# Kernel optimization log

Hardware: AMD Instinct MI355X
Metric: run time of the kernel (lower is better)

The kernel has to match this reference:

```python
import jax, jax.numpy as jnp
import numpy as np

S, T, BERT, POS = 256, 512, 768, 128
H1 = 1024
NUM_CLASSES = 6


def setup_inputs() -> dict:
    key = jax.random.key(0)
    ks = jax.random.split(key, 12)
    emb = jax.random.normal(ks[0], (S, T, BERT), dtype=jnp.float32)
    pos = jax.random.normal(ks[1], (S, T, POS), dtype=jnp.float32)
    seg = jnp.sort(jax.random.randint(ks[2], (S,), 0, 64)).astype(jnp.int32)
    scale = 0.02
    return {
        "embeddings": emb,
        "position_encodings": pos,
        "W_attn": jax.random.normal(ks[3], (BERT + POS, 1), dtype=jnp.float32) * scale,
        "b_attn": jnp.zeros((1,), dtype=jnp.float32),
        "W1": jax.random.normal(ks[4], (BERT, H1), dtype=jnp.float32) * scale,
        "b1": jnp.zeros((H1,), dtype=jnp.float32),
        "W2": jax.random.normal(ks[5], (H1, H1), dtype=jnp.float32) * scale,
        "b2": jnp.zeros((H1,), dtype=jnp.float32),
        "W3": jax.random.normal(ks[6], (H1, NUM_CLASSES), dtype=jnp.float32) * scale,
        "b3": jnp.zeros((NUM_CLASSES,), dtype=jnp.float32),
        "segment_ids": seg,
        "num_comments": 64,
    }


def reference(embeddings, position_encodings, W_attn, b_attn, W1, b1, W2, b2, W3, b3, segment_ids, num_comments):
    # attention logits: Linear(bert+pos -> 1) over concatenated features, shape (S, T, 1)
    attn = jnp.concatenate([embeddings, position_encodings], axis=2) @ W_attn + b_attn
    # per-segment softmax over the 512-token dim (torch Softmax(1) on (b-a, 512, 1))
    w = jax.nn.softmax(attn, axis=1)
    # softmax-weighted pooling per segment -> (S, BERT)
    segvec = jnp.sum(w * embeddings, axis=1)
    # ragged sum over each comment's segments (contiguous bounds == sorted segment ids)
    vecs = jax.ops.segment_sum(segvec, segment_ids, num_segments=num_comments)
    # MLP head with LeakyReLU (torch default slope 0.01) and Sigmoid
    h = jax.nn.leaky_relu(vecs @ W1 + b1, negative_slope=0.01)
    h = jax.nn.leaky_relu(h @ W2 + b2, negative_slope=0.01)
    return jax.nn.sigmoid(h @ W3 + b3)
```

## Files before the change

### kernel.cpp

```cpp
#include <hip/hip_runtime.h>
#include <math.h>
#include <stdint.h>

#define S_SEQ 256
#define T_TOK 512
#define BERT 768
#define POSD 128
#define H1 1024
#define NC 6

#define CHUNK_T 128
#define WTOK 32

__global__ __launch_bounds__(256, 4) void pool_kernel(
    const float* __restrict__ emb, const float* __restrict__ pos,
    const float* __restrict__ Wa, const float* __restrict__ ba,
    float* __restrict__ part_acc, float* __restrict__ part_ml)
{
    __shared__ float mg[4 * BERT];
    __shared__ float wml[8];

    const int tid = threadIdx.x;
    const int w   = tid >> 6;
    const int l   = tid & 63;
    const int b   = blockIdx.x;
    const int s   = b >> 2;
    const int t0  = (b & 3) * CHUNK_T + w * WTOK;

    const float4* Wa4 = (const float4*)Wa;
    const float4 wa0 = Wa4[l];
    const float4 wa1 = Wa4[64 + l];
    const float4 wa2 = Wa4[128 + l];
    const float2 wp  = ((const float2*)(Wa + BERT))[l];
    const float  bav = ba[0];

    const float4* erow = (const float4*)(emb + ((size_t)s * T_TOK + t0) * BERT);
    const float2* prow = (const float2*)(pos + ((size_t)s * T_TOK + t0) * POSD);

    float m = -INFINITY, lsum = 0.f;
    float acc[12];
    #pragma unroll
    for (int j = 0; j < 12; ++j) acc[j] = 0.f;

    for (int i = 0; i < WTOK; i += 2) {
        const float4* r0 = erow + i * (BERT / 4);
        const float4* r1 = r0 + (BERT / 4);
        const float4 a0 = r0[l], a1 = r0[64 + l], a2 = r0[128 + l];
        const float4 b0 = r1[l], b1 = r1[64 + l], b2 = r1[128 + l];
        const float2 q0 = prow[i * (POSD / 2) + l];
        const float2 q1 = prow[(i + 1) * (POSD / 2) + l];

        float d0 = a0.x*wa0.x + a0.y*wa0.y + a0.z*wa0.z + a0.w*wa0.w
                 + a1.x*wa1.x + a1.y*wa1.y + a1.z*wa1.z + a1.w*wa1.w
                 + a2.x*wa2.x + a2.y*wa2.y + a2.z*wa2.z + a2.w*wa2.w
                 + q0.x*wp.x  + q0.y*wp.y;
        float d1 = b0.x*wa0.x + b0.y*wa0.y + b0.z*wa0.z + b0.w*wa0.w
                 + b1.x*wa1.x + b1.y*wa1.y + b1.z*wa1.z + b1.w*wa1.w
                 + b2.x*wa2.x + b2.y*wa2.y + b2.z*wa2.z + b2.w*wa2.w
                 + q1.x*wp.x  + q1.y*wp.y;
        #pragma unroll
        for (int off = 32; off >= 1; off >>= 1) {
            d0 += __shfl_xor(d0, off, 64);
            d1 += __shfl_xor(d1, off, 64);
        }

        const float lg0 = d0 + bav;
        const float lg1 = d1 + bav;
        const float mn  = fmaxf(m, fmaxf(lg0, lg1));
        const float alpha = __expf(m - mn);
        const float p0 = __expf(lg0 - mn);
        const float p1 = __expf(lg1 - mn);
        lsum = lsum * alpha + p0 + p1;
        m = mn;

        acc[0]  = fmaf(p0, a0.x, fmaf(p1, b0.x, acc[0]  * alpha));
        acc[1]  = fmaf(p0, a0.y, fmaf(p1, b0.y, acc[1]  * alpha));
        acc[2]  = fmaf(p0, a0.z, fmaf(p1, b0.z, acc[2]  * alpha));
        acc[3]  = fmaf(p0, a0.w, fmaf(p1, b0.w, acc[3]  * alpha));
        acc[4]  = fmaf(p0, a1.x, fmaf(p1, b1.x, acc[4]  * alpha));
        acc[5]  = fmaf(p0, a1.y, fmaf(p1, b1.y, acc[5]  * alpha));
        acc[6]  = fmaf(p0, a1.z, fmaf(p1, b1.z, acc[6]  * alpha));
        acc[7]  = fmaf(p0, a1.w, fmaf(p1, b1.w, acc[7]  * alpha));
        acc[8]  = fmaf(p0, a2.x, fmaf(p1, b2.x, acc[8]  * alpha));
        acc[9]  = fmaf(p0, a2.y, fmaf(p1, b2.y, acc[9]  * alpha));
        acc[10] = fmaf(p0, a2.z, fmaf(p1, b2.z, acc[10] * alpha));
        acc[11] = fmaf(p0, a2.w, fmaf(p1, b2.w, acc[11] * alpha));
    }

    #pragma unroll
    for (int j = 0; j < 4; ++j) {
        mg[w * BERT +       l * 4 + j] = acc[j];
        mg[w * BERT + 256 + l * 4 + j] = acc[4 + j];
        mg[w * BERT + 512 + l * 4 + j] = acc[8 + j];
    }
    if (l == 0) { wml[w * 2] = m; wml[w * 2 + 1] = lsum; }
    __syncthreads();

    const float m0 = wml[0], l0 = wml[1], m1 = wml[2], l1 = wml[3];
    const float m2 = wml[4], l2 = wml[5], m3 = wml[6], l3 = wml[7];
    const float M  = fmaxf(fmaxf(m0, m1), fmaxf(m2, m3));
    const float e0 = __expf(m0 - M), e1 = __expf(m1 - M);
    const float e2 = __expf(m2 - M), e3 = __expf(m3 - M);
    const float lt = l0 * e0 + l1 * e1 + l2 * e2 + l3 * e3;
    #pragma unroll
    for (int k = 0; k < 3; ++k) {
        const int col = tid * 3 + k;
        part_acc[(size_t)b * BERT + col] =
              e0 * mg[col] + e1 * mg[BERT + col]
            + e2 * mg[2 * BERT + col] + e3 * mg[3 * BERT + col];
    }
    if (tid == 0) { part_ml[b * 2] = M; part_ml[b * 2 + 1] = lt; }
}

__global__ void combine_segsum(
    const float* __restrict__ part_acc, const float* __restrict__ part_ml,
    const int* __restrict__ seg, float* __restrict__ vecs)
{
    const int c = blockIdx.x;
    const int tid = threadIdx.x;
    float v0 = 0.f, v1 = 0.f, v2 = 0.f;
    for (int s = 0; s < S_SEQ; ++s) {
        if (seg[s] != c) continue;
        const int p = s * 4;
        const float m0 = part_ml[(p+0)*2], l0 = part_ml[(p+0)*2+1];
        const float m1 = part_ml[(p+1)*2], l1 = part_ml[(p+1)*2+1];
        const float m2 = part_ml[(p+2)*2], l2 = part_ml[(p+2)*2+1];
        const float m3 = part_ml[(p+3)*2], l3 = part_ml[(p+3)*2+1];
        const float M  = fmaxf(fmaxf(m0, m1), fmaxf(m2, m3));
        const float e0 = __expf(m0 - M), e1 = __expf(m1 - M);
        const float e2 = __expf(m2 - M), e3 = __expf(m3 - M);
        const float inv = 1.0f / (l0*e0 + l1*e1 + l2*e2 + l3*e3);
        const int col = tid * 3;
        v0 += inv * (e0 * part_acc[(size_t)(p+0)*BERT + col]
                   + e1 * part_acc[(size_t)(p+1)*BERT + col]
                   + e2 * part_acc[(size_t)(p+2)*BERT + col]
                   + e3 * part_acc[(size_t)(p+3)*BERT + col]);
        v1 += inv * (e0 * part_acc[(size_t)(p+0)*BERT + col + 1]
                   + e1 * part_acc[(size_t)(p+1)*BERT + col + 1]
                   + e2 * part_acc[(size_t)(p+2)*BERT + col + 1]
                   + e3 * part_acc[(size_t)(p+3)*BERT + col + 1]);
        v2 += inv * (e0 * part_acc[(size_t)(p+0)*BERT + col + 2]
                   + e1 * part_acc[(size_t)(p+1)*BERT + col + 2]
                   + e2 * part_acc[(size_t)(p+2)*BERT + col + 2]
                   + e3 * part_acc[(size_t)(p+3)*BERT + col + 2]);
    }
    vecs[(size_t)c*BERT + tid*3 + 0] = v0;
    vecs[(size_t)c*BERT + tid*3 + 1] = v1;
    vecs[(size_t)c*BERT + tid*3 + 2] = v2;
}

__global__ void mlp_layer(
    const float* __restrict__ in, const float* __restrict__ W,
    const float* __restrict__ bias, float* __restrict__ out, int K)
{
    __shared__ float v[H1];
    const int c  = blockIdx.y;
    const int tid = threadIdx.x;
    const int j  = blockIdx.x * 256 + tid;
    for (int i = tid; i < K; i += 256) v[i] = in[(size_t)c*K + i];
    __syncthreads();
    float a0 = 0.f, a1 = 0.f, a2 = 0.f, a3 = 0.f;
    #pragma unroll 4
    for (int k = 0; k < K; k += 4) {
        a0 = fmaf(v[k  ], W[(size_t)(k  )*H1 + j], a0);
        a1 = fmaf(v[k+1], W[(size_t)(k+1)*H1 + j], a1);
        a2 = fmaf(v[k+2], W[(size_t)(k+2)*H1 + j], a2);
        a3 = fmaf(v[k+3], W[(size_t)(k+3)*H1 + j], a3);
    }
    const float acc = bias[j] + ((a0 + a1) + (a2 + a3));
    out[(size_t)c*H1 + j] = acc > 0.f ? acc : 0.01f * acc;
}

__global__ void mlp_out(
    const float* __restrict__ h, const float* __restrict__ W3,
    const float* __restrict__ b3, float* __restrict__ out)
{
    __shared__ float v[H1];
    __shared__ float red[NC][4];
    const int c = blockIdx.x;
    const int tid = threadIdx.x;
    const int wave = tid >> 6, lane = tid & 63;
    for (int i = tid; i < H1; i += 256) v[i] = h[(size_t)c * H1 + i];
    __syncthreads();
    float po[NC] = {0.f, 0.f, 0.f, 0.f, 0.f, 0.f};
    for (int k = tid; k < H1; k += 256) {
        const float hv = v[k];
        #pragma unroll
        for (int o = 0; o < NC; ++o) po[o] = fmaf(hv, W3[k * NC + o], po[o]);
    }
    #pragma unroll
    for (int o = 0; o < NC; ++o) {
        float d = po[o];
        #pragma unroll
        for (int off = 32; off >= 1; off >>= 1) d += __shfl_xor(d, off, 64);
        if (lane == 0) red[o][wave] = d;
    }
    __syncthreads();
    if (tid < NC) {
        const float sum = red[tid][0] + red[tid][1] + red[tid][2] + red[tid][3] + b3[tid];
        out[c * NC + tid] = 1.0f / (1.0f + __expf(-sum));
    }
}

extern "C" void kernel_launch(void* const* d_in, const int* in_sizes, int n_in,
                              void* d_out, int out_size, void* d_ws, size_t ws_size,
                              hipStream_t stream)
{
    const float* emb = (const float*)d_in[0];
    const float* pos = (const float*)d_in[1];
    const float* Wa  = (const float*)d_in[2];
    const float* ba  = (const float*)d_in[3];
    const float* W1  = (const float*)d_in[4];
    const float* b1  = (const float*)d_in[5];
    const float* W2  = (const float*)d_in[6];
    const float* b2  = (const float*)d_in[7];
    const float* W3  = (const float*)d_in[8];
    const float* b3  = (const float*)d_in[9];
    const int*   seg = (const int*)d_in[10];
    float* out = (float*)d_out;

    float* ws = (float*)d_ws;
    float* part_acc = ws;
    float* part_ml  = part_acc + 1024 * BERT;
    float* vecs     = part_ml  + 1024 * 2;
    float* h1       = vecs     + 64 * BERT;
    float* h2       = h1       + 64 * H1;

    pool_kernel<<<1024, 256, 0, stream>>>(emb, pos, Wa, ba, part_acc, part_ml);
    combine_segsum<<<64, 256, 0, stream>>>(part_acc, part_ml, seg, vecs);
    mlp_layer<<<dim3(4, 64), 256, 0, stream>>>(vecs, W1, b1, h1, BERT);
    mlp_layer<<<dim3(4, 64), 256, 0, stream>>>(h1, W2, b2, h2, H1);
    mlp_out<<<64, 256, 0, stream>>>(h2, W3, b3, out);
}
```

Baseline: 677.1 us.

## Prefetch pool rows, use DPP wave reduction, split-K MLP layers with atomics

The pool kernel now software-pipelines its loads, fetching the next two token rows while the current pair is processed, and it replaces the shuffle-based wave reduction with DPP row shifts plus permlane swaps. The MLP layers are split four ways along K over a 3D grid and accumulate with atomicAdd into outputs that combine_segsum pre-fills with the bias. LeakyReLU is moved to where the next layer reads its input. This adds parallelism to the small MLP launches, at the cost of atomics, nondeterministic summation order, and more register pressure in the pool kernel.

```diff
diff --git a/kernel.cpp b/kernel.cpp
--- a/kernel.cpp
+++ b/kernel.cpp
@@ -12,6 +12,23 @@
 #define CHUNK_T 128
 #define WTOK 32
 
+__device__ __forceinline__ float wave_sum64(float x) {
+    x += __int_as_float(__builtin_amdgcn_update_dpp(
+            0, __float_as_int(x), 0x128, 0xF, 0xF, true));
+    x += __int_as_float(__builtin_amdgcn_update_dpp(
+            0, __float_as_int(x), 0x124, 0xF, 0xF, true));
+    x += __int_as_float(__builtin_amdgcn_update_dpp(
+            0, __float_as_int(x), 0x122, 0xF, 0xF, true));
+    x += __int_as_float(__builtin_amdgcn_update_dpp(
+            0, __float_as_int(x), 0x121, 0xF, 0xF, true));
+    float a = x, b = x;
+    asm("v_permlane16_swap_b32 %0, %1" : "+v"(a), "+v"(b));
+    x = a + b;
+    a = x; b = x;
+    asm("v_permlane32_swap_b32 %0, %1" : "+v"(a), "+v"(b));
+    return a + b;
+}
+
 __global__ __launch_bounds__(256, 4) void pool_kernel(
     const float* __restrict__ emb, const float* __restrict__ pos,
     const float* __restrict__ Wa, const float* __restrict__ ba,
@@ -42,13 +59,22 @@
     #pragma unroll
     for (int j = 0; j < 12; ++j) acc[j] = 0.f;
 
+    float4 na0 = erow[l],       na1 = erow[64 + l],  na2 = erow[128 + l];
+    float4 nb0 = erow[192 + l], nb1 = erow[256 + l], nb2 = erow[320 + l];
+    float2 nq0 = prow[l],       nq1 = prow[64 + l];
+
     for (int i = 0; i < WTOK; i += 2) {
-        const float4* r0 = erow + i * (BERT / 4);
-        const float4* r1 = r0 + (BERT / 4);
-        const float4 a0 = r0[l], a1 = r0[64 + l], a2 = r0[128 + l];
-        const float4 b0 = r1[l], b1 = r1[64 + l], b2 = r1[128 + l];
-        const float2 q0 = prow[i * (POSD / 2) + l];
-        const float2 q1 = prow[(i + 1) * (POSD / 2) + l];
+        const float4 a0 = na0, a1 = na1, a2 = na2;
+        const float4 b0 = nb0, b1 = nb1, b2 = nb2;
+        const float2 q0 = nq0, q1 = nq1;
+
+        if (i + 2 < WTOK) {
+            const float4* rn = erow + (size_t)(i + 2) * (BERT / 4);
+            na0 = rn[l];       na1 = rn[64 + l];  na2 = rn[128 + l];
+            nb0 = rn[192 + l]; nb1 = rn[256 + l]; nb2 = rn[320 + l];
+            nq0 = prow[(i + 2) * (POSD / 2) + l];
+            nq1 = prow[(i + 3) * (POSD / 2) + l];
+        }
 
         float d0 = a0.x*wa0.x + a0.y*wa0.y + a0.z*wa0.z + a0.w*wa0.w
                  + a1.x*wa1.x + a1.y*wa1.y + a1.z*wa1.z + a1.w*wa1.w
@@ -58,11 +84,9 @@
                  + b1.x*wa1.x + b1.y*wa1.y + b1.z*wa1.z + b1.w*wa1.w
                  + b2.x*wa2.x + b2.y*wa2.y + b2.z*wa2.z + b2.w*wa2.w
                  + q1.x*wp.x  + q1.y*wp.y;
-        #pragma unroll
-        for (int off = 32; off >= 1; off >>= 1) {
-            d0 += __shfl_xor(d0, off, 64);
-            d1 += __shfl_xor(d1, off, 64);
-        }
+
+        d0 = wave_sum64(d0);
+        d1 = wave_sum64(d1);
 
         const float lg0 = d0 + bav;
         const float lg1 = d1 + bav;
@@ -114,10 +138,18 @@
 
 __global__ void combine_segsum(
     const float* __restrict__ part_acc, const float* __restrict__ part_ml,
-    const int* __restrict__ seg, float* __restrict__ vecs)
+    const int* __restrict__ seg, float* __restrict__ vecs,
+    const float* __restrict__ b1, const float* __restrict__ b2,
+    float* __restrict__ h1, float* __restrict__ h2)
 {
     const int c = blockIdx.x;
     const int tid = threadIdx.x;
+
+    for (int j = tid; j < H1; j += 256) {
+        h1[(size_t)c * H1 + j] = b1[j];
+        h2[(size_t)c * H1 + j] = b2[j];
+    }
+
     float v0 = 0.f, v1 = 0.f, v2 = 0.f;
     for (int s = 0; s < S_SEQ; ++s) {
         if (seg[s] != c) continue;
@@ -149,26 +181,34 @@
     vecs[(size_t)c*BERT + tid*3 + 2] = v2;
 }
 
-__global__ void mlp_layer(
+__global__ __launch_bounds__(256) void mlp_layer_part(
     const float* __restrict__ in, const float* __restrict__ W,
-    const float* __restrict__ bias, float* __restrict__ out, int K)
-{
-    __shared__ float v[H1];
-    const int c  = blockIdx.y;
-    const int tid = threadIdx.x;
-    const int j  = blockIdx.x * 256 + tid;
-    for (int i = tid; i < K; i += 256) v[i] = in[(size_t)c*K + i];
-    __syncthreads();
+    float* __restrict__ out, int K, int lr_in)
+{
+    __shared__ float v[256];
+    const int c      = blockIdx.y;
+    const int kchunk = K >> 2;
+    const int k0     = blockIdx.z * kchunk;
+    const int tid    = threadIdx.x;
+    const int j      = blockIdx.x * 256 + tid;
+
+    if (tid < kchunk) {
+        float x = in[(size_t)c * K + k0 + tid];
+        if (lr_in) x = x > 0.f ? x : 0.01f * x;
+        v[tid] = x;
+    }
+    __syncthreads();
+
     float a0 = 0.f, a1 = 0.f, a2 = 0.f, a3 = 0.f;
+    const float* Wp = W + (size_t)k0 * H1 + j;
     #pragma unroll 4
-    for (int k = 0; k < K; k += 4) {
-        a0 = fmaf(v[k  ], W[(size_t)(k  )*H1 + j], a0);
-        a1 = fmaf(v[k+1], W[(size_t)(k+1)*H1 + j], a1);
-        a2 = fmaf(v[k+2], W[(size_t)(k+2)*H1 + j], a2);
-        a3 = fmaf(v[k+3], W[(size_t)(k+3)*H1 + j], a3);
-    }
-    const float acc = bias[j] + ((a0 + a1) + (a2 + a3));
-    out[(size_t)c*H1 + j] = acc > 0.f ? acc : 0.01f * acc;
+    for (int k = 0; k < kchunk; k += 4) {
+        a0 = fmaf(v[k    ], Wp[(size_t)(k    ) * H1], a0);
+        a1 = fmaf(v[k + 1], Wp[(size_t)(k + 1) * H1], a1);
+        a2 = fmaf(v[k + 2], Wp[(size_t)(k + 2) * H1], a2);
+        a3 = fmaf(v[k + 3], Wp[(size_t)(k + 3) * H1], a3);
+    }
+    atomicAdd(&out[(size_t)c * H1 + j], (a0 + a1) + (a2 + a3));
 }
 
 __global__ void mlp_out(
@@ -180,7 +220,10 @@
     const int c = blockIdx.x;
     const int tid = threadIdx.x;
     const int wave = tid >> 6, lane = tid & 63;
-    for (int i = tid; i < H1; i += 256) v[i] = h[(size_t)c * H1 + i];
+    for (int i = tid; i < H1; i += 256) {
+        float x = h[(size_t)c * H1 + i];
+        v[i] = x > 0.f ? x : 0.01f * x;
+    }
     __syncthreads();
     float po[NC] = {0.f, 0.f, 0.f, 0.f, 0.f, 0.f};
     for (int k = tid; k < H1; k += 256) {
@@ -227,8 +270,9 @@
     float* h2       = h1       + 64 * H1;
 
     pool_kernel<<<1024, 256, 0, stream>>>(emb, pos, Wa, ba, part_acc, part_ml);
-    combine_segsum<<<64, 256, 0, stream>>>(part_acc, part_ml, seg, vecs);
-    mlp_layer<<<dim3(4, 64), 256, 0, stream>>>(vecs, W1, b1, h1, BERT);
-    mlp_layer<<<dim3(4, 64), 256, 0, stream>>>(h1, W2, b2, h2, H1);
+    combine_segsum<<<64, 256, 0, stream>>>(part_acc, part_ml, seg, vecs,
+                                           b1, b2, h1, h2);
+    mlp_layer_part<<<dim3(4, 64, 4), 256, 0, stream>>>(vecs, W1, h1, BERT, 0);
+    mlp_layer_part<<<dim3(4, 64, 4), 256, 0, stream>>>(h1, W2, h2, H1, 1);
     mlp_out<<<64, 256, 0, stream>>>(h2, W3, b3, out);
 }
```

Result: faster. 629.8 us (-7.0%).
